# Performance work log

Hardware: AMD Instinct MI355X
Metric: run time of the kernel (lower is better)

The kernel has to match this reference:

```python
import jax, jax.numpy as jnp
import numpy as np
from jax import lax

DN = ('NHWC', 'HWIO', 'NHWC')

def _conv(a, w):
    return lax.conv_general_dilated(a, w, (1, 1), 'SAME', dimension_numbers=DN)

def _hard_sigmoid(z):
    return jnp.clip(0.2 * z + 0.5, 0.0, 1.0)


def setup_inputs() -> dict:
    key = jax.random.key(0)
    ks = jax.random.split(key, 4)
    B, T, H, W, C, F, K = 2, 16, 64, 64, 64, 64, 3
    x = jax.random.normal(ks[0], (B, T, H, W, C), dtype=jnp.float32)
    Wx = jax.random.normal(ks[1], (K, K, C, 4 * F), dtype=jnp.float32) * (2.0 / (K * K * C)) ** 0.5
    Wh = jax.random.normal(ks[2], (K, K, F, 4 * F), dtype=jnp.float32) * (2.0 / (K * K * F)) ** 0.5
    b = jax.random.normal(ks[3], (4 * F,), dtype=jnp.float32) * 0.01
    gamma = jnp.ones((F,), dtype=jnp.float32)
    beta = jnp.zeros((F,), dtype=jnp.float32)
    moving_mean = jnp.zeros((F,), dtype=jnp.float32)
    moving_var = jnp.ones((F,), dtype=jnp.float32)
    return {"x": x, "Wx": Wx, "Wh": Wh, "b": b, "gamma": gamma,
            "beta": beta, "moving_mean": moving_mean, "moving_var": moving_var}


def reference(x, Wx, Wh, b, gamma, beta, moving_mean, moving_var):
    B, T, H, W, C = x.shape
    F = Wh.shape[2]
    # Precompute the input-to-gate convolutions for all timesteps in one big conv.
    xg = _conv(x.reshape(B * T, H, W, C), Wx) + b          # (B*T, H, W, 4F)
    xg = xg.reshape(B, T, H, W, 4 * F).transpose(1, 0, 2, 3, 4)  # (T, B, H, W, 4F)

    h0 = jnp.zeros((B, H, W, F), dtype=x.dtype)
    c0 = jnp.zeros((B, H, W, F), dtype=x.dtype)

    def step(carry, xt):
        h, c = carry
        z = xt + _conv(h, Wh)                               # (B, H, W, 4F)
        zi, zf, zg, zo = jnp.split(z, 4, axis=-1)           # Keras gate order: i, f, c, o
        i = _hard_sigmoid(zi)
        f = _hard_sigmoid(zf)
        g = jnp.tanh(zg)
        o = _hard_sigmoid(zo)
        c_new = f * c + i * g
        h_new = o * jnp.tanh(c_new)
        return (h_new, c_new), h_new

    _, hs = lax.scan(step, (h0, c0), xg)                    # (T, B, H, W, F)
    out = hs.transpose(1, 0, 2, 3, 4)                       # (B, T, H, W, F)

    # BatchNormalization in inference mode (training=False), eps=1e-3 (Keras default)
    eps = 1e-3
    inv = gamma * lax.rsqrt(moving_var + eps)
    out = out * inv + (beta - moving_mean * inv)
    return out
```

## Files before the change

### kernel.cpp

```cpp
#include <hip/hip_runtime.h>
#include <cstddef>

typedef __attribute__((ext_vector_type(8))) _Float16 half8;
typedef __attribute__((ext_vector_type(4))) float f32x4;
typedef __attribute__((ext_vector_type(4))) unsigned short us4;

#define TT 16
#define APAD 72
#define A_TILE (3*34*APAD)
#define B_OFF  (2*A_TILE)
#define CHUNK  8192
#define NCHUNK 36
#define NBUF   6
#define PFDIST 5

__device__ __forceinline__ unsigned short f2h(float f) {
    return __builtin_bit_cast(unsigned short, (_Float16)f);
}
__device__ __forceinline__ float hsig(float z) {
    return fminf(fmaxf(0.2f * z + 0.5f, 0.f), 1.f);
}

typedef __attribute__((address_space(3))) unsigned int lds_uint;
typedef const __attribute__((address_space(1))) unsigned int glb_uint;
__device__ __forceinline__ void async16(const void* g, void* l) {
    __builtin_amdgcn_global_load_lds((glb_uint*)g, (lds_uint*)l, 16, 0, 0);
}

#define WAITVM(N) { asm volatile("s_waitcnt vmcnt(" #N ")" ::: "memory"); \
                    __builtin_amdgcn_sched_barrier(0); }

__global__ __launch_bounds__(256) void prep_kernel(
    const float* __restrict__ Wx, const float* __restrict__ Wh,
    const float* __restrict__ gamma, const float* __restrict__ beta,
    const float* __restrict__ mean, const float* __restrict__ var,
    unsigned short* __restrict__ Wc, float* __restrict__ bn)
{
    if (blockIdx.x == 1152) {
        if (threadIdx.x < 64) {
            const int c = threadIdx.x;
            const float inv = gamma[c] * rsqrtf(var[c] + 1e-3f);
            bn[c] = inv;
            bn[64 + c] = beta[c] - mean[c] * inv;
        }
        return;
    }
    const int i = blockIdx.x * 256 + threadIdx.x;
    const int j  = i & 7;
    const int n  = (i >> 3) & 255;
    const int kg = (i >> 11) & 3;
    const int s  = i >> 13;
    const int sub = s % 18;
    const float* W = (s >= 18) ? Wh : Wx;
    const int k5 = sub * 32 + kg * 8 + j;
    const int c = k5 & 63, q = k5 >> 6;
    const int kx = q % 3, ky = q / 3;
    Wc[i] = f2h(W[(size_t)((ky * 3 + kx) * 64 + c) * 256 + n]);
}

template<int PASS>
__device__ __forceinline__ void conv_pass(
    const unsigned short* __restrict__ Wc,
    const int soff0, const int soff1,
    unsigned short* lds0, unsigned short* lds1,
    const unsigned short* abase,
    const unsigned short* bbase,
    f32x4 acc[2][2])
{
    #pragma unroll
    for (int sub = 0; sub < 18; ++sub) {
        const int ci = PASS * 18 + sub;
        if (ci + PFDIST < NCHUNK) {
            const int sc = ci + PFDIST;
            const unsigned short* gsc = Wc + (size_t)sc * CHUNK;
            const int bsel = (sc % NBUF) * CHUNK;
            async16(gsc + soff0, lds0 + bsel);
            async16(gsc + soff1, lds1 + bsel);
        }
        const int rem = NCHUNK - 1 - ci;
        if (rem >= PFDIST) WAITVM(10)
        else if (rem == 4) WAITVM(8)
        else if (rem == 3) WAITVM(6)
        else if (rem == 2) WAITVM(4)
        else if (rem == 1) WAITVM(2)
        else               WAITVM(0)

        const int ky = sub / 6, kx = (sub / 2) % 3, cb = sub & 1;
        const int aimm = (ky * 34 + kx) * APAD + cb * 32;
        const unsigned short* bbuf = bbase + (ci % NBUF) * CHUNK;

        const half8 b0 = *(const half8*)(bbuf);
        const half8 b1 = *(const half8*)(bbuf + 128);
        const unsigned short* at = abase + PASS * A_TILE + aimm;
        const half8 a0 = *(const half8*)(at);
        const half8 a1 = *(const half8*)(at + 16 * APAD);
        acc[0][0] = __builtin_amdgcn_mfma_f32_16x16x32_f16(a0, b0, acc[0][0], 0, 0, 0);
        acc[0][1] = __builtin_amdgcn_mfma_f32_16x16x32_f16(a0, b1, acc[0][1], 0, 0, 0);
        acc[1][0] = __builtin_amdgcn_mfma_f32_16x16x32_f16(a1, b0, acc[1][0], 0, 0, 0);
        acc[1][1] = __builtin_amdgcn_mfma_f32_16x16x32_f16(a1, b1, acc[1][1], 0, 0, 0);
    }
}

__global__ __launch_bounds__(512) void convstep_kernel(
    const float* __restrict__ x,
    const unsigned short* __restrict__ hb,
    const unsigned short* __restrict__ Wc,
    const float* __restrict__ bias,
    float* __restrict__ cbuf,
    unsigned short* __restrict__ ho,
    const float* __restrict__ bn,
    float* __restrict__ out,
    const int t)
{
    const int bid0 = blockIdx.x;
    const int bid = (bid0 & 7) * 32 + (bid0 >> 3);
    const int xh = bid & 1;
    const int y  = (bid >> 1) & 63;
    const int n  = bid >> 7;
    const int tid = threadIdx.x;
    const int lane = tid & 63;
    const int w = tid >> 6;

    __shared__ __align__(16) unsigned short smem[B_OFF + NBUF * CHUNK];

    const float* __restrict__ xt = x + (size_t)(n * TT + t) * 4096 * 64;
    const size_t hbase = (size_t)n * 4096 * 64;
    for (int idx = tid; idx < 2 * 3 * 34 * 8; idx += 512) {
        const int cg  = idx & 7;
        const int col = (idx >> 3) % 34;
        const int i3  = (idx >> 3) / 34;
        const int r   = i3 % 3;
        const int src = i3 / 3;
        const int gy = y + r - 1;
        const int gx = xh * 32 + col - 1;
        const bool ok = ((unsigned)gy < 64u) && ((unsigned)gx < 64u);
        const int ebase = (r * 34 + col) * APAD + cg * 8;
        if (src == 0) {
            float4 v0 = make_float4(0.f, 0.f, 0.f, 0.f), v1 = v0;
            if (ok) {
                const float* p = xt + (size_t)(gy * 64 + gx) * 64 + cg * 8;
                v0 = *(const float4*)p;
                v1 = *(const float4*)(p + 4);
            }
            us4 h0, h1;
            h0.x = f2h(v0.x); h0.y = f2h(v0.y); h0.z = f2h(v0.z); h0.w = f2h(v0.w);
            h1.x = f2h(v1.x); h1.y = f2h(v1.y); h1.z = f2h(v1.z); h1.w = f2h(v1.w);
            *(us4*)&smem[ebase]     = h0;
            *(us4*)&smem[ebase + 4] = h1;
        } else {
            uint4 v = make_uint4(0u, 0u, 0u, 0u);
            if (ok) v = *(const uint4*)(hb + hbase + (size_t)(gy * 64 + gx) * 64 + cg * 8);
            *(uint4*)&smem[A_TILE + ebase] = v;
        }
    }

    const int soff0 = ((lane >> 5)    ) * 2048 + (w * 32 + (lane & 31)) * 8;
    const int soff1 = ((lane >> 5) + 2) * 2048 + (w * 32 + (lane & 31)) * 8;
    unsigned short* lds0 = smem + B_OFF + w * 1024 + (lane     ) * 8;
    unsigned short* lds1 = smem + B_OFF + w * 1024 + (64 + lane) * 8;

    #pragma unroll
    for (int sc = 0; sc < PFDIST; ++sc) {
        const unsigned short* gsc = Wc + (size_t)sc * CHUNK;
        async16(gsc + soff0, lds0 + sc * CHUNK);
        async16(gsc + soff1, lds1 + sc * CHUNK);
    }
    __syncthreads();

    const int p0 = lane & 15;
    const int g  = lane >> 4;
    const unsigned short* abase = smem + p0 * APAD + g * 8;
    const unsigned short* bbase = smem + B_OFF + w * 1024 + (g * 32 + p0) * 8;

    f32x4 acc[2][2] = {};
    conv_pass<0>(Wc, soff0, soff1, lds0, lds1, abase, bbase, acc);
    conv_pass<1>(Wc, soff0, soff1, lds0, lds1, abase, bbase, acc);

    __syncthreads();
    float* gbuf = (float*)smem;
    const int gate = w >> 1;
    const int chalf = (w & 1) * 32;

    float bv[2];
    bv[0] = bias[w * 32 + p0];
    bv[1] = bias[w * 32 + 16 + p0];

    #pragma unroll
    for (int mf = 0; mf < 2; ++mf)
        #pragma unroll
        for (int nf = 0; nf < 2; ++nf)
            #pragma unroll
            for (int j = 0; j < 4; ++j) {
                float v = acc[mf][nf][j] + bv[nf];
                v = (gate == 2) ? tanhf(v) : hsig(v);
                const int px = mf * 16 + g * 4 + j;
                gbuf[(gate * 32 + px) * 68 + chalf + nf * 16 + p0] = v;
            }
    __syncthreads();

    const int p  = tid >> 4;
    const int c4 = (tid & 15) * 4;
    const float4 iv = *(const float4*)&gbuf[(0 * 32 + p) * 68 + c4];
    const float4 fv = *(const float4*)&gbuf[(1 * 32 + p) * 68 + c4];
    const float4 gv = *(const float4*)&gbuf[(2 * 32 + p) * 68 + c4];
    const float4 ov = *(const float4*)&gbuf[(3 * 32 + p) * 68 + c4];
    const size_t gpix = (size_t)((n * 64 + y) * 64 + xh * 32 + p);
    const size_t sb = gpix * 64 + c4;
    const float4 cold = *(const float4*)&cbuf[sb];
    const float4 scv  = *(const float4*)&bn[c4];
    const float4 shv  = *(const float4*)&bn[64 + c4];

    const float ivv[4] = {iv.x, iv.y, iv.z, iv.w};
    const float fvv[4] = {fv.x, fv.y, fv.z, fv.w};
    const float gvv[4] = {gv.x, gv.y, gv.z, gv.w};
    const float ovv[4] = {ov.x, ov.y, ov.z, ov.w};
    const float cov[4] = {cold.x, cold.y, cold.z, cold.w};
    const float scc[4] = {scv.x, scv.y, scv.z, scv.w};
    const float shh[4] = {shv.x, shv.y, shv.z, shv.w};

    float cnew[4], obuf[4];
    us4 hh;
    unsigned short* hhp = (unsigned short*)&hh;
    #pragma unroll
    for (int j = 0; j < 4; ++j) {
        const float cn = fvv[j] * cov[j] + ivv[j] * gvv[j];
        const float hn = ovv[j] * tanhf(cn);
        cnew[j] = cn;
        hhp[j] = f2h(hn);
        obuf[j] = hn * scc[j] + shh[j];
    }
    *(float4*)&cbuf[sb] = *(float4*)&cnew[0];
    *(us4*)&ho[sb]      = hh;
    const size_t ob = ((size_t)((n * TT + t) * 4096 + y * 64 + xh * 32 + p)) * 64 + c4;
    *(float4*)&out[ob] = *(float4*)&obuf[0];
}

extern "C" void kernel_launch(void* const* d_in, const int* in_sizes, int n_in,
                              void* d_out, int out_size, void* d_ws, size_t ws_size,
                              hipStream_t stream) {
    const float* x     = (const float*)d_in[0];
    const float* Wx    = (const float*)d_in[1];
    const float* Wh    = (const float*)d_in[2];
    const float* b     = (const float*)d_in[3];
    const float* gamma = (const float*)d_in[4];
    const float* beta  = (const float*)d_in[5];
    const float* mean  = (const float*)d_in[6];
    const float* var   = (const float*)d_in[7];
    float* out = (float*)d_out;
    char* ws = (char*)d_ws;

    unsigned short* Wc   = (unsigned short*)(ws);
    float*          bn   = (float*)(ws + 589824);
    unsigned short* hA   = (unsigned short*)(ws + 590336);
    float*          cbuf = (float*)(ws + 1638912);
    unsigned short* hB   = (unsigned short*)(ws + 3736064);

    hipMemsetAsync(ws + 590336, 0, 3145728, stream);
    prep_kernel<<<1153, 256, 0, stream>>>(Wx, Wh, gamma, beta, mean, var, Wc, bn);

    for (int t = 0; t < TT; ++t) {
        const bool even = (t & 1) == 0;
        convstep_kernel<<<256, 512, 0, stream>>>(
            x,
            even ? hA : hB,
            Wc, b, cbuf,
            even ? hB : hA,
            bn, out, t);
    }
}
```

Baseline: 216.6 us.

## Precompute input-gate convolution for all timesteps in one parallel kernel

Adds an xconv kernel that computes the input-to-gate convolution plus bias for all timesteps at once, using 2048 blocks, and stores the result as fp16 in the workspace. Each per-step kernel then runs only the 18 recurrent-weight chunks and adds the precomputed xg values. This takes half of the MFMA work and the x-tile staging off the serial critical path. In exchange it uses 64MB of extra workspace and an fp16 round trip of the gate preactivations, which adds rounding. If the workspace is too small, it falls back to the fused path.

```diff
diff --git a/kernel.cpp b/kernel.cpp
--- a/kernel.cpp
+++ b/kernel.cpp
@@ -8,14 +8,16 @@
 #define TT 16
 #define APAD 72
 #define A_TILE (3*34*APAD)
-#define B_OFF  (2*A_TILE)
+#define XA_TILE (3*66*APAD)
 #define CHUNK  8192
-#define NCHUNK 36
 #define NBUF   6
 #define PFDIST 5
 
 __device__ __forceinline__ unsigned short f2h(float f) {
     return __builtin_bit_cast(unsigned short, (_Float16)f);
+}
+__device__ __forceinline__ float h2f(unsigned short u) {
+    return (float)__builtin_bit_cast(_Float16, u);
 }
 __device__ __forceinline__ float hsig(float z) {
     return fminf(fmaxf(0.2f * z + 0.5f, 0.f), 1.f);
@@ -58,8 +60,8 @@
     Wc[i] = f2h(W[(size_t)((ky * 3 + kx) * 64 + c) * 256 + n]);
 }
 
-template<int PASS>
-__device__ __forceinline__ void conv_pass(
+template<int C0, int CLAST, int AOFF>
+__device__ __forceinline__ void conv_pass18(
     const unsigned short* __restrict__ Wc,
     const int soff0, const int soff1,
     unsigned short* lds0, unsigned short* lds1,
@@ -69,15 +71,15 @@
 {
     #pragma unroll
     for (int sub = 0; sub < 18; ++sub) {
-        const int ci = PASS * 18 + sub;
-        if (ci + PFDIST < NCHUNK) {
+        const int ci = C0 + sub;
+        if (ci + PFDIST <= CLAST) {
             const int sc = ci + PFDIST;
             const unsigned short* gsc = Wc + (size_t)sc * CHUNK;
             const int bsel = (sc % NBUF) * CHUNK;
             async16(gsc + soff0, lds0 + bsel);
             async16(gsc + soff1, lds1 + bsel);
         }
-        const int rem = NCHUNK - 1 - ci;
+        const int rem = CLAST - ci;
         if (rem >= PFDIST) WAITVM(10)
         else if (rem == 4) WAITVM(8)
         else if (rem == 3) WAITVM(6)
@@ -91,7 +93,7 @@
 
         const half8 b0 = *(const half8*)(bbuf);
         const half8 b1 = *(const half8*)(bbuf + 128);
-        const unsigned short* at = abase + PASS * A_TILE + aimm;
+        const unsigned short* at = abase + AOFF + aimm;
         const half8 a0 = *(const half8*)(at);
         const half8 a1 = *(const half8*)(at + 16 * APAD);
         acc[0][0] = __builtin_amdgcn_mfma_f32_16x16x32_f16(a0, b0, acc[0][0], 0, 0, 0);
@@ -101,11 +103,111 @@
     }
 }
 
+__global__ __launch_bounds__(512) void xconv_kernel(
+    const float* __restrict__ x,
+    const unsigned short* __restrict__ Wc,
+    const float* __restrict__ bias,
+    unsigned short* __restrict__ xg)
+{
+    const int bid = blockIdx.x;
+    const int y = bid & 63;
+    const int t = (bid >> 6) & 15;
+    const int n = bid >> 10;
+    const int tid = threadIdx.x, lane = tid & 63, w = tid >> 6;
+
+    __shared__ __align__(16) unsigned short smem[XA_TILE + NBUF * CHUNK];
+
+    const int soff0 = ((lane >> 5)    ) * 2048 + (w * 32 + (lane & 31)) * 8;
+    const int soff1 = ((lane >> 5) + 2) * 2048 + (w * 32 + (lane & 31)) * 8;
+    unsigned short* lds0 = smem + XA_TILE + w * 1024 + (lane     ) * 8;
+    unsigned short* lds1 = smem + XA_TILE + w * 1024 + (64 + lane) * 8;
+    #pragma unroll
+    for (int sc = 0; sc < PFDIST; ++sc) {
+        const unsigned short* gsc = Wc + (size_t)sc * CHUNK;
+        async16(gsc + soff0, lds0 + sc * CHUNK);
+        async16(gsc + soff1, lds1 + sc * CHUNK);
+    }
+
+    const float* __restrict__ xt = x + (size_t)(n * TT + t) * 4096 * 64;
+    for (int idx = tid; idx < 3 * 66 * 8; idx += 512) {
+        const int cg  = idx & 7;
+        const int col = (idx >> 3) % 66;
+        const int r   = (idx >> 3) / 66;
+        const int gy = y + r - 1;
+        const int gx = col - 1;
+        const bool ok = ((unsigned)gy < 64u) && ((unsigned)gx < 64u);
+        float4 v0 = make_float4(0.f, 0.f, 0.f, 0.f), v1 = v0;
+        if (ok) {
+            const float* p = xt + (size_t)(gy * 64 + gx) * 64 + cg * 8;
+            v0 = *(const float4*)p;
+            v1 = *(const float4*)(p + 4);
+        }
+        us4 h0, h1;
+        h0.x = f2h(v0.x); h0.y = f2h(v0.y); h0.z = f2h(v0.z); h0.w = f2h(v0.w);
+        h1.x = f2h(v1.x); h1.y = f2h(v1.y); h1.z = f2h(v1.z); h1.w = f2h(v1.w);
+        const int ebase = (r * 66 + col) * APAD + cg * 8;
+        *(us4*)&smem[ebase]     = h0;
+        *(us4*)&smem[ebase + 4] = h1;
+    }
+    __syncthreads();
+
+    const int p0 = lane & 15, g = lane >> 4;
+    const unsigned short* abase = smem + p0 * APAD + g * 8;
+    const unsigned short* bbase = smem + XA_TILE + w * 1024 + (g * 32 + p0) * 8;
+
+    f32x4 acc[4][2] = {};
+    #pragma unroll
+    for (int sub = 0; sub < 18; ++sub) {
+        if (sub + PFDIST < 18) {
+            const int sc = sub + PFDIST;
+            const unsigned short* gsc = Wc + (size_t)sc * CHUNK;
+            const int bsel = (sc % NBUF) * CHUNK;
+            async16(gsc + soff0, lds0 + bsel);
+            async16(gsc + soff1, lds1 + bsel);
+        }
+        const int rem = 17 - sub;
+        if (rem >= PFDIST) WAITVM(10)
+        else if (rem == 4) WAITVM(8)
+        else if (rem == 3) WAITVM(6)
+        else if (rem == 2) WAITVM(4)
+        else if (rem == 1) WAITVM(2)
+        else               WAITVM(0)
+
+        const int ky = sub / 6, kx = (sub / 2) % 3, cb = sub & 1;
+        const unsigned short* bbuf = bbase + (sub % NBUF) * CHUNK;
+        const half8 b0 = *(const half8*)(bbuf);
+        const half8 b1 = *(const half8*)(bbuf + 128);
+        #pragma unroll
+        for (int mf = 0; mf < 4; ++mf) {
+            const half8 a = *(const half8*)(abase + (ky * 66 + kx + mf * 16) * APAD + cb * 32);
+            acc[mf][0] = __builtin_amdgcn_mfma_f32_16x16x32_f16(a, b0, acc[mf][0], 0, 0, 0);
+            acc[mf][1] = __builtin_amdgcn_mfma_f32_16x16x32_f16(a, b1, acc[mf][1], 0, 0, 0);
+        }
+    }
+
+    const size_t obase = ((size_t)((n * TT + t) * 4096 + y * 64)) * 256;
+    const float bv0 = bias[w * 32 + p0];
+    const float bv1 = bias[w * 32 + 16 + p0];
+    #pragma unroll
+    for (int mf = 0; mf < 4; ++mf)
+        #pragma unroll
+        for (int nf = 0; nf < 2; ++nf) {
+            const float bv = nf ? bv1 : bv0;
+            #pragma unroll
+            for (int j = 0; j < 4; ++j) {
+                const int px = mf * 16 + g * 4 + j;
+                xg[obase + (size_t)px * 256 + w * 32 + nf * 16 + p0] = f2h(acc[mf][nf][j] + bv);
+            }
+        }
+}
+
+template<int FUSED>
 __global__ __launch_bounds__(512) void convstep_kernel(
     const float* __restrict__ x,
     const unsigned short* __restrict__ hb,
     const unsigned short* __restrict__ Wc,
     const float* __restrict__ bias,
+    const unsigned short* __restrict__ xg,
     float* __restrict__ cbuf,
     unsigned short* __restrict__ ho,
     const float* __restrict__ bn,
@@ -120,12 +222,40 @@
     const int tid = threadIdx.x;
     const int lane = tid & 63;
     const int w = tid >> 6;
-
-    __shared__ __align__(16) unsigned short smem[B_OFF + NBUF * CHUNK];
+    const int p0 = lane & 15;
+    const int g  = lane >> 4;
+
+    constexpr int NTILE = FUSED ? 2 : 1;
+    constexpr int BOFF  = NTILE * A_TILE;
+    __shared__ __align__(16) unsigned short smem[NTILE * A_TILE + NBUF * CHUNK];
+
+    unsigned short xgv[2][2][4];
+    if (!FUSED) {
+        const size_t xb = ((size_t)((n * TT + t) * 4096 + y * 64 + xh * 32)) * 256 + w * 32;
+        #pragma unroll
+        for (int mf = 0; mf < 2; ++mf)
+            #pragma unroll
+            for (int nf = 0; nf < 2; ++nf)
+                #pragma unroll
+                for (int j = 0; j < 4; ++j)
+                    xgv[mf][nf][j] = xg[xb + (size_t)(mf * 16 + g * 4 + j) * 256 + nf * 16 + p0];
+    }
+
+    constexpr int C0 = FUSED ? 0 : 18;
+    const int soff0 = ((lane >> 5)    ) * 2048 + (w * 32 + (lane & 31)) * 8;
+    const int soff1 = ((lane >> 5) + 2) * 2048 + (w * 32 + (lane & 31)) * 8;
+    unsigned short* lds0 = smem + BOFF + w * 1024 + (lane     ) * 8;
+    unsigned short* lds1 = smem + BOFF + w * 1024 + (64 + lane) * 8;
+    #pragma unroll
+    for (int sc = C0; sc < C0 + PFDIST; ++sc) {
+        const unsigned short* gsc = Wc + (size_t)sc * CHUNK;
+        async16(gsc + soff0, lds0 + (sc % NBUF) * CHUNK);
+        async16(gsc + soff1, lds1 + (sc % NBUF) * CHUNK);
+    }
 
     const float* __restrict__ xt = x + (size_t)(n * TT + t) * 4096 * 64;
     const size_t hbase = (size_t)n * 4096 * 64;
-    for (int idx = tid; idx < 2 * 3 * 34 * 8; idx += 512) {
+    for (int idx = tid; idx < NTILE * 3 * 34 * 8; idx += 512) {
         const int cg  = idx & 7;
         const int col = (idx >> 3) % 34;
         const int i3  = (idx >> 3) / 34;
@@ -135,7 +265,7 @@
         const int gx = xh * 32 + col - 1;
         const bool ok = ((unsigned)gy < 64u) && ((unsigned)gx < 64u);
         const int ebase = (r * 34 + col) * APAD + cg * 8;
-        if (src == 0) {
+        if (FUSED && src == 0) {
             float4 v0 = make_float4(0.f, 0.f, 0.f, 0.f), v1 = v0;
             if (ok) {
                 const float* p = xt + (size_t)(gy * 64 + gx) * 64 + cg * 8;
@@ -150,31 +280,21 @@
         } else {
             uint4 v = make_uint4(0u, 0u, 0u, 0u);
             if (ok) v = *(const uint4*)(hb + hbase + (size_t)(gy * 64 + gx) * 64 + cg * 8);
-            *(uint4*)&smem[A_TILE + ebase] = v;
-        }
-    }
-
-    const int soff0 = ((lane >> 5)    ) * 2048 + (w * 32 + (lane & 31)) * 8;
-    const int soff1 = ((lane >> 5) + 2) * 2048 + (w * 32 + (lane & 31)) * 8;
-    unsigned short* lds0 = smem + B_OFF + w * 1024 + (lane     ) * 8;
-    unsigned short* lds1 = smem + B_OFF + w * 1024 + (64 + lane) * 8;
-
-    #pragma unroll
-    for (int sc = 0; sc < PFDIST; ++sc) {
-        const unsigned short* gsc = Wc + (size_t)sc * CHUNK;
-        async16(gsc + soff0, lds0 + sc * CHUNK);
-        async16(gsc + soff1, lds1 + sc * CHUNK);
+            *(uint4*)&smem[(FUSED ? A_TILE : 0) + ebase] = v;
+        }
     }
     __syncthreads();
 
-    const int p0 = lane & 15;
-    const int g  = lane >> 4;
     const unsigned short* abase = smem + p0 * APAD + g * 8;
-    const unsigned short* bbase = smem + B_OFF + w * 1024 + (g * 32 + p0) * 8;
+    const unsigned short* bbase = smem + BOFF + w * 1024 + (g * 32 + p0) * 8;
 
     f32x4 acc[2][2] = {};
-    conv_pass<0>(Wc, soff0, soff1, lds0, lds1, abase, bbase, acc);
-    conv_pass<1>(Wc, soff0, soff1, lds0, lds1, abase, bbase, acc);
+    if (FUSED) {
+        conv_pass18<0, 35, 0>(Wc, soff0, soff1, lds0, lds1, abase, bbase, acc);
+        conv_pass18<18, 35, A_TILE>(Wc, soff0, soff1, lds0, lds1, abase, bbase, acc);
+    } else {
+        conv_pass18<18, 35, 0>(Wc, soff0, soff1, lds0, lds1, abase, bbase, acc);
+    }
 
     __syncthreads();
     float* gbuf = (float*)smem;
@@ -191,7 +311,7 @@
         for (int nf = 0; nf < 2; ++nf)
             #pragma unroll
             for (int j = 0; j < 4; ++j) {
-                float v = acc[mf][nf][j] + bv[nf];
+                float v = acc[mf][nf][j] + (FUSED ? bv[nf] : h2f(xgv[mf][nf][j]));
                 v = (gate == 2) ? tanhf(v) : hsig(v);
                 const int px = mf * 16 + g * 4 + j;
                 gbuf[(gate * 32 + px) * 68 + chalf + nf * 16 + p0] = v;
@@ -254,17 +374,24 @@
     unsigned short* hA   = (unsigned short*)(ws + 590336);
     float*          cbuf = (float*)(ws + 1638912);
     unsigned short* hB   = (unsigned short*)(ws + 3736064);
+    unsigned short* xg   = (unsigned short*)(ws + 4784640);
+    const size_t NEED = 4784640ull + 67108864ull;
 
     hipMemsetAsync(ws + 590336, 0, 3145728, stream);
     prep_kernel<<<1153, 256, 0, stream>>>(Wx, Wh, gamma, beta, mean, var, Wc, bn);
 
-    for (int t = 0; t < TT; ++t) {
-        const bool even = (t & 1) == 0;
-        convstep_kernel<<<256, 512, 0, stream>>>(
-            x,
-            even ? hA : hB,
-            Wc, b, cbuf,
-            even ? hB : hA,
-            bn, out, t);
-    }
-}
+    if (ws_size >= NEED) {
+        xconv_kernel<<<2048, 512, 0, stream>>>(x, Wc, b, xg);
+        for (int t = 0; t < TT; ++t) {
+            const bool even = (t & 1) == 0;
+            convstep_kernel<0><<<256, 512, 0, stream>>>(
+                x, even ? hA : hB, Wc, b, xg, cbuf, even ? hB : hA, bn, out, t);
+        }
+    } else {
+        for (int t = 0; t < TT; ++t) {
+            const bool even = (t & 1) == 0;
+            convstep_kernel<1><<<256, 512, 0, stream>>>(
+                x, even ? hA : hB, Wc, b, xg, cbuf, even ? hB : hA, bn, out, t);
+        }
+    }
+}
```

After: 212.5 us. Within noise of the previous version (-1.9%).
